# Kernel tuning notes

Hardware: AMD Instinct MI355X
Metric: run time of the kernel (lower is better)

The kernel has to match this reference:

```python
import math
import jax, jax.numpy as jnp
import numpy as np

EPS = 1e-4
FMAX = 18  # max filtersize for scale clamped to 2.5: ceil(3*2^2.5+0.5)=18 -> kernel 37x37
KSZ = 2 * FMAX + 1


def _conv2d(x, w, b):
    # 3x3 conv, padding 1, NCHW / OIHW (cross-correlation, matches torch)
    y = jax.lax.conv_general_dilated(x, w, (1, 1), [(1, 1), (1, 1)],
                                     dimension_numbers=('NCHW', 'OIHW', 'NCHW'))
    return y + b[None, :, None, None]


def _basis_filters(scale):
    # scale: [B] -> [B,3,K,K] (g, dgdx, dgdy), masked to the per-sample support
    std = 2.0 ** scale                              # [B]
    fs = jnp.ceil(3.0 * std + 0.5)                  # per-sample filtersize
    x = jnp.arange(-FMAX, FMAX + 1, dtype=jnp.float32)          # [K]
    m = (jnp.abs(x)[None, :] <= fs[:, None]).astype(jnp.float32)  # [B,K] support mask
    e = jnp.exp(-0.5 * (x[None, :] / std[:, None]) ** 2) * m      # masked 1D gaussian [B,K]
    g = e[:, :, None] * e[:, None, :]                              # [B,K,K]
    g = g / jnp.sum(g, axis=(1, 2), keepdims=True)
    c = (-x[None, :] / (std[:, None] ** 3 * 2.0 * math.pi)) * e    # [B,K]
    dgdx = c[:, :, None] * e[:, None, :]   # varies along first spatial dim (x[0])
    dgdx = dgdx / jnp.sum(jnp.abs(dgdx), axis=(1, 2), keepdims=True)
    dgdy = e[:, :, None] * c[:, None, :]   # varies along second spatial dim (x[1])
    dgdy = dgdy / jnp.sum(jnp.abs(dgdy), axis=(1, 2), keepdims=True)
    return jnp.stack([g, dgdx, dgdy], axis=1)  # [B,3,K,K]


def setup_inputs() -> dict:
    key = jax.random.key(0)
    ks = jax.random.split(key, 7)
    B, H, W = 8, 512, 512
    batch = jax.random.uniform(ks[0], (B, 3, H, W), dtype=jnp.float32)
    gcm = jnp.array([[0.06, 0.63, 0.27], [0.3, 0.04, -0.35], [0.34, -0.6, 0.17]],
                    dtype=jnp.float32)
    w1 = jax.random.normal(ks[1], (16, 3, 3, 3), dtype=jnp.float32) * 0.1
    b1 = jax.random.normal(ks[2], (16,), dtype=jnp.float32) * 0.01
    w2 = jax.random.normal(ks[3], (16, 16, 3, 3), dtype=jnp.float32) * 0.1
    b2 = jax.random.normal(ks[4], (16,), dtype=jnp.float32) * 0.01
    w3 = jax.random.normal(ks[5], (1, 16, 3, 3), dtype=jnp.float32) * 0.1
    b3 = jax.random.normal(ks[6], (1,), dtype=jnp.float32) * 0.01
    return {"batch": batch, "gcm": gcm, "w1": w1, "b1": b1,
            "w2": w2, "b2": b2, "w3": w3, "b3": b3}


def reference(batch, gcm, w1, b1, w2, b2, w3, b3):
    B, _, H, W = batch.shape
    # ---- RGB order prior (non-differentiable, no_grad in torch) ----
    oh = lambda i: jax.nn.one_hot(i, 3, axis=1, dtype=batch.dtype)
    mx = jnp.argmax(batch, axis=1)                 # first max
    mn = jnp.argmin(batch, axis=1)
    bf = batch[:, ::-1]
    mx2 = 2 - jnp.argmax(bf, axis=1)               # last max
    mn2 = 2 - jnp.argmin(bf, axis=1)
    RGB_order = jax.lax.stop_gradient(
        0.5 * (oh(mx) + oh(mx2)) - 0.5 * (oh(mn) + oh(mn2)))  # [B,3,H,W]

    # ---- per-sample adaptive scale from small CNN ----
    h = jax.nn.silu(_conv2d(batch, w1, b1))
    h = jax.nn.silu(_conv2d(h, w2, b2))
    s = _conv2d(h, w3, b3)
    scale = jnp.clip(jnp.mean(s, axis=(1, 2, 3)), -2.5, 2.5)   # [B]

    # ---- Gaussian color model ----
    xg = jnp.einsum('ij,bjhw->bihw', gcm, batch)  # [B,3,H,W] -> (E, El, Ell)

    # ---- per-sample Gaussian basis convolution, batched via grouped conv ----
    basis = _basis_filters(scale)                                  # [B,3,K,K]
    xin = xg.reshape(1, B * 3, H, W)
    wk = jnp.broadcast_to(basis[:, None], (B, 3, 3, KSZ, KSZ)).reshape(B * 9, 1, KSZ, KSZ)
    out = jax.lax.conv_general_dilated(xin, wk, (1, 1), [(FMAX, FMAX), (FMAX, FMAX)],
                                       feature_group_count=B * 3,
                                       dimension_numbers=('NCHW', 'OIHW', 'NCHW'))
    out = out.reshape(B, 3, 3, H, W)   # [B, chan(E/El/Ell), filt(g/dx/dy), H, W]
    E = out[:, 0, 0:1]
    Ex = out[:, 0, 1:2]
    Ey = out[:, 0, 2:3]
    El = out[:, 1, 0:1]
    Ell = out[:, 2, 0:1]

    Hf = jnp.arctan(El / (Ell + EPS))
    S = jnp.log((El ** 2 + Ell ** 2) / (E ** 2 + EPS) + EPS)
    Ww = jnp.arctan((Ex / (E + EPS)) ** 2 + (Ey / (E + EPS)) ** 2)
    return jnp.concatenate([Hf, S, RGB_order, Ww], axis=1)  # [B,6,H,W]
```

## Files before the change

### kernel.cpp

```cpp
#include <hip/hip_runtime.h>
#include <hip/hip_bf16.h>

constexpr int BN = 8, HH = 512, WW = 512;
constexpr int PIX = HH * WW;
constexpr float EPSF = 1e-4f;

__device__ __forceinline__ float b2f(__hip_bfloat16 x) { return __bfloat162float(x); }
__device__ __forceinline__ __hip_bfloat16 f2b(float x) { return __float2bfloat16(x); }
__device__ __forceinline__ unsigned short bfbits(float x) {
    union { __hip_bfloat16 b; unsigned short u; } cv; cv.b = f2b(x); return cv.u;
}

typedef __attribute__((ext_vector_type(8))) short bf16x8;
typedef __attribute__((ext_vector_type(4))) float f32x4;

constexpr int OFF_TOT = 0;
constexpr int OFF_ROW0 = 128;
constexpr int OFF_ROW1 = 256;
constexpr int OFF_COL0 = 384;
constexpr int OFF_COL1 = 512;
constexpr int OFF_COR = 640;
constexpr int OFF_WR  = 2048;
constexpr int OFF_EH  = 4608;
constexpr int OFF_CH  = 5120;
constexpr size_t OFF_TPB = 65536;
constexpr size_t TP_BYTES = (size_t)4 * BN * PIX * 4;
constexpr size_t WS_NEEDED = OFF_TPB + TP_BYTES;

__global__ void prep_kernel(const float* __restrict__ w2, float* __restrict__ wsf) {
    int t = threadIdx.x;
    for (int i = t; i < 640; i += 256) wsf[i] = 0.f;
    unsigned short* ab = (unsigned short*)(wsf + OFF_WR);
    for (int idx = t; idx < 5120; idx += 256) {
        int part = idx / 2560;
        int id = idx - part * 2560;
        int ks = id >> 9, rem = id & 511, lane = rem >> 3, j = id & 7;
        int oc = lane & 15, q = lane >> 4;
        int k = q * 8 + j;
        int tap = 2 * ks + (k >> 4), ic = k & 15;
        float val = (tap <= 8) ? w2[oc * 144 + ic * 9 + tap] : 0.f;
        float hv = b2f(f2b(val));
        ab[idx] = (part == 0) ? bfbits(val) : bfbits(val - hv);
    }
}

__device__ __forceinline__ void conv1_px(const float v[27], const float* __restrict__ w1,
                                         const float* __restrict__ b1, unsigned int u[8]) {
    float o[16];
#pragma unroll
    for (int oc = 0; oc < 16; oc++) {
        float a = b1[oc];
#pragma unroll
        for (int j = 0; j < 27; j++) a += v[j] * w1[oc * 27 + j];
        o[oc] = a / (1.f + __expf(-a));
    }
#pragma unroll
    for (int k = 0; k < 8; k++)
        u[k] = (unsigned int)bfbits(o[2 * k]) | ((unsigned int)bfbits(o[2 * k + 1]) << 16);
}

__global__ __launch_bounds__(256) void conv12_kernel(const float* __restrict__ batch,
                                                     const float* __restrict__ w1,
                                                     const float* __restrict__ b1,
                                                     const unsigned short* __restrict__ abuf,
                                                     const float* __restrict__ b2v,
                                                     const float* __restrict__ gcm,
                                                     float* __restrict__ wsf,
                                                     float* __restrict__ out) {
    __shared__ uint4 h1s[18 * 66 * 2];
    __shared__ float part[4][16];

    int tx = threadIdx.x;
    int lane = tx & 63, wave = tx >> 6;
    int n = lane & 15, q = lane >> 4;
    int w0 = blockIdx.x * 64, h0 = blockIdx.y * 16, b = blockIdx.z;
    bool edge = (blockIdx.x == 0) || (blockIdx.x == 7) || (blockIdx.y == 0) || (blockIdx.y == 31);

    union { uint4 u; bf16x8 v; } cv;
    bf16x8 ah[5], al[5];
    const uint4* ab4 = (const uint4*)abuf;
#pragma unroll
    for (int ks = 0; ks < 5; ks++) {
        cv.u = ab4[ks * 64 + lane];       ah[ks] = cv.v;
        cv.u = ab4[320 + ks * 64 + lane]; al[ks] = cv.v;
    }

    const float* pb = batch + (size_t)(b * 3) * PIX;
    for (int i = tx; i < 18 * 66; i += 256) {
        int r = i / 66, c = i - r * 66;
        int gh = h0 - 1 + r, gw = w0 - 1 + c;
        unsigned int u[8];
        if (!edge) {
            const float* p0 = pb + (size_t)(gh - 1) * WW + (gw - 1);
            float v[27];
#pragma unroll
            for (int ic = 0; ic < 3; ic++)
#pragma unroll
                for (int kh = 0; kh < 3; kh++)
#pragma unroll
                    for (int kw = 0; kw < 3; kw++)
                        v[ic * 9 + kh * 3 + kw] = p0[(size_t)ic * PIX + kh * WW + kw];
            conv1_px(v, w1, b1, u);
        } else if (gh >= 0 && gh < HH && gw >= 0 && gw < WW) {
            float v[27];
#pragma unroll
            for (int ic = 0; ic < 3; ic++) {
                const float* p = pb + (size_t)ic * PIX;
#pragma unroll
                for (int kh = 0; kh < 3; kh++) {
                    int hh = gh + kh - 1;
#pragma unroll
                    for (int kw = 0; kw < 3; kw++) {
                        int ww = gw + kw - 1;
                        float x = 0.f;
                        if (hh >= 0 && hh < HH && ww >= 0 && ww < WW) x = p[hh * WW + ww];
                        v[ic * 9 + kh * 3 + kw] = x;
                    }
                }
            }
            conv1_px(v, w1, b1, u);
        } else {
#pragma unroll
            for (int k = 0; k < 8; k++) u[k] = 0u;
        }
        int swz = (c >> 2) & 1;
        int base = i * 2;
        h1s[base + swz]       = make_uint4(u[0], u[1], u[2], u[3]);
        h1s[base + (swz ^ 1)] = make_uint4(u[4], u[5], u[6], u[7]);
    }

    for (int j = tx; j < 1024; j += 256) {
        int rr = j >> 6, ccx = j & 63;
        size_t p = (size_t)(h0 + rr) * WW + (w0 + ccx);
        float v0 = pb[p], v1 = pb[(size_t)PIX + p], v2 = pb[2 * (size_t)PIX + p];
        int mx  = (v0 >= v1 && v0 >= v2) ? 0 : ((v1 >= v2) ? 1 : 2);
        int mx2 = (v2 >= v1 && v2 >= v0) ? 2 : ((v1 >= v0) ? 1 : 0);
        int mn  = (v0 <= v1 && v0 <= v2) ? 0 : ((v1 <= v2) ? 1 : 2);
        int mn2 = (v2 <= v1 && v2 <= v0) ? 2 : ((v1 <= v0) ? 1 : 0);
#pragma unroll
        for (int c = 0; c < 3; c++) {
            float r = 0.5f * ((float)(c == mx) + (float)(c == mx2))
                    - 0.5f * ((float)(c == mn) + (float)(c == mn2));
            out[(size_t)(b * 6 + 2 + c) * PIX + p] = r;
        }
    }
    __syncthreads();

    float tt[4] = {0, 0, 0, 0};
    float cs0[4] = {0, 0, 0, 0};
    float cs1[4] = {0, 0, 0, 0};
    for (int rloc = 0; rloc < 4; rloc++) {
        int row = wave * 4 + rloc;
        int grow = h0 + row;
        f32x4 acc[4] = {{0,0,0,0},{0,0,0,0},{0,0,0,0},{0,0,0,0}};
#pragma unroll
        for (int ks = 0; ks < 5; ks++) {
            int tap = 2 * ks + (q >> 1); if (tap > 8) tap = 8;
            int dh = tap / 3 - 1, dw = tap % 3 - 1;
            int half = q & 1;
            int lr = row + 1 + dh;
#pragma unroll
            for (int t = 0; t < 4; t++) {
                int c = 1 + dw + t * 16 + n;
                cv.u = h1s[(lr * 66 + c) * 2 + (half ^ ((c >> 2) & 1))];
                acc[t] = __builtin_amdgcn_mfma_f32_16x16x32_bf16(ah[ks], cv.v, acc[t], 0, 0, 0);
                acc[t] = __builtin_amdgcn_mfma_f32_16x16x32_bf16(al[ks], cv.v, acc[t], 0, 0, 0);
            }
        }
        float sv[4][4];
#pragma unroll
        for (int t = 0; t < 4; t++)
#pragma unroll
            for (int r = 0; r < 4; r++) {
                float a = acc[t][r] + b2v[q * 4 + r];
                sv[t][r] = a / (1.f + __expf(-a));
            }
#pragma unroll
        for (int r = 0; r < 4; r++) tt[r] += sv[0][r] + sv[1][r] + sv[2][r] + sv[3][r];
        if (grow == 0 || grow == HH - 1) {
            int off = (grow == 0) ? OFF_ROW0 : OFF_ROW1;
#pragma unroll
            for (int r = 0; r < 4; r++) {
                float x = sv[0][r] + sv[1][r] + sv[2][r] + sv[3][r];
#pragma unroll
                for (int d = 1; d < 16; d <<= 1) x += __shfl_xor(x, d, 64);
                if (n == 0) atomicAdd(&wsf[off + b * 16 + q * 4 + r], x);
            }
        }
        if (blockIdx.x == 0 && n == 0)
#pragma unroll
            for (int r = 0; r < 4; r++) cs0[r] += sv[0][r];
        if (blockIdx.x == 7 && n == 15)
#pragma unroll
            for (int r = 0; r < 4; r++) cs1[r] += sv[3][r];
        if ((grow == 0 || grow == HH - 1)) {
            int hi = (grow == 0) ? 0 : 1;
            if (blockIdx.x == 0 && n == 0)
#pragma unroll
                for (int r = 0; r < 4; r++)
                    wsf[OFF_COR + ((b * 2 + hi) * 2 + 0) * 16 + q * 4 + r] = sv[0][r];
            if (blockIdx.x == 7 && n == 15)
#pragma unroll
                for (int r = 0; r < 4; r++)
                    wsf[OFF_COR + ((b * 2 + hi) * 2 + 1) * 16 + q * 4 + r] = sv[3][r];
        }
    }
    if (blockIdx.x == 0 && n == 0)
#pragma unroll
        for (int r = 0; r < 4; r++) atomicAdd(&wsf[OFF_COL0 + b * 16 + q * 4 + r], cs0[r]);
    if (blockIdx.x == 7 && n == 15)
#pragma unroll
        for (int r = 0; r < 4; r++) atomicAdd(&wsf[OFF_COL1 + b * 16 + q * 4 + r], cs1[r]);
#pragma unroll
    for (int r = 0; r < 4; r++) {
        float x = tt[r];
#pragma unroll
        for (int d = 1; d < 16; d <<= 1) x += __shfl_xor(x, d, 64);
        tt[r] = x;
    }
    if (n == 0)
#pragma unroll
        for (int r = 0; r < 4; r++) part[wave][q * 4 + r] = tt[r];
    __syncthreads();
    if (tx < 16)
        atomicAdd(&wsf[OFF_TOT + b * 16 + tx],
                  part[0][tx] + part[1][tx] + part[2][tx] + part[3][tx]);
}

__global__ void filter_kernel(const float* __restrict__ w3, const float* __restrict__ b3,
                              float* __restrict__ wsf) {
    int b = blockIdx.x, t = threadIdx.x;
    __shared__ float red[160];
    float val = 0.f;
    if (t < 144) {
        int ic = t / 9, tap = t % 9, kh = tap / 3, kw = tap % 3;
        float T = wsf[OFF_TOT + b * 16 + ic];
        int hi = -1, wi = -1;
        if (kh == 0) { T -= wsf[OFF_ROW1 + b * 16 + ic]; hi = 1; }
        else if (kh == 2) { T -= wsf[OFF_ROW0 + b * 16 + ic]; hi = 0; }
        if (kw == 0) { T -= wsf[OFF_COL1 + b * 16 + ic]; wi = 1; }
        else if (kw == 2) { T -= wsf[OFF_COL0 + b * 16 + ic]; wi = 0; }
        if (hi >= 0 && wi >= 0) T += wsf[OFF_COR + ((b * 2 + hi) * 2 + wi) * 16 + ic];
        val = w3[t] * T;
    }
    red[t] = val;
    __syncthreads();
    __shared__ float sh_mean;
    if (t == 0) {
        float S = 0.f;
        for (int i = 0; i < 144; i++) S += red[i];
        sh_mean = b3[0] + S * (1.f / (float)PIX);
    }
    __syncthreads();
    float scale = fminf(2.5f, fmaxf(-2.5f, sh_mean));
    float sd = exp2f(scale);
    float fs = ceilf(3.f * sd + 0.5f);
    float e = 0.f, c = 0.f;
    if (t < 37) {
        float x = (float)(t - 18);
        if (fabsf(x) <= fs) {
            float qq = x / sd;
            e = __expf(-0.5f * qq * qq);
            c = -x / (sd * sd * sd * 6.28318530717958647692f) * e;
        }
    }
    __shared__ float sa[40], sb[40];
    if (t < 37) { sa[t] = e; sb[t] = fabsf(c); }
    __syncthreads();
    __shared__ float Se, Sc;
    if (t == 0) {
        float a = 0.f, d = 0.f;
        for (int i = 0; i < 37; i++) { a += sa[i]; d += sb[i]; }
        Se = a; Sc = d;
    }
    __syncthreads();
    if (t < 37) {
        wsf[OFF_EH + b * 37 + t] = e / Se;
        wsf[OFF_CH + b * 37 + t] = c / Sc;
    }
}

__device__ __forceinline__ int skw(int c) { return c + (c >> 5); }
__global__ __launch_bounds__(256, 4) void horiz_kernel(const float* __restrict__ batch,
                                                       const float* __restrict__ gcm,
                                                       const float* __restrict__ ehat,
                                                       const float* __restrict__ chat,
                                                       float* __restrict__ t) {
    __shared__ float xr[2][3][566];
    int tx = threadIdx.x;
    int h0 = blockIdx.x * 2;
    int b  = blockIdx.y;
    const float* pb = batch + (size_t)(b * 3) * PIX;
    float g0 = gcm[0], g1 = gcm[1], g2 = gcm[2];
    float g3 = gcm[3], g4 = gcm[4], g5 = gcm[5];
    float g6 = gcm[6], g7 = gcm[7], g8 = gcm[8];
    for (int i = tx; i < 2 * 548; i += 256) {
        int r = i / 548, c = i - r * 548;
        int gw = c - 18;
        float v0 = 0.f, v1 = 0.f, v2 = 0.f;
        if (gw >= 0 && gw < WW) {
            size_t p = (size_t)(h0 + r) * WW + gw;
            v0 = pb[p]; v1 = pb[(size_t)PIX + p]; v2 = pb[2 * (size_t)PIX + p];
        }
        int cs = skw(c);
        xr[r][0][cs] = g0 * v0 + g1 * v1 + g2 * v2;
        xr[r][1][cs] = g3 * v0 + g4 * v1 + g5 * v2;
        xr[r][2][cs] = g6 * v0 + g7 * v1 + g8 * v2;
    }
    __syncthreads();
    int r = tx >> 7, colbase = (tx & 127) * 4;
    const float* eh = ehat + b * 37; const float* ch = chat + b * 37;
    float a0[4] = {}, a1[4] = {}, a2[4] = {}, a3[4] = {};
#pragma unroll 4
    for (int kk = 0; kk < 40; kk++) {
        int cs = skw(colbase + kk);
        float x0 = xr[r][0][cs], x1 = xr[r][1][cs], x2 = xr[r][2][cs];
#pragma unroll
        for (int i = 0; i < 4; i++) {
            int k = kk - i;
            if (k >= 0 && k < 37) {
                float ce = eh[k], cc = ch[k];
                a0[i] += ce * x0; a1[i] += ce * x1;
                a2[i] += ce * x2; a3[i] += cc * x0;
            }
        }
    }
    const size_t PL = (size_t)BN * PIX;
    size_t p = (size_t)b * PIX + (size_t)(h0 + r) * WW + colbase;
    *(float4*)&t[0 * PL + p] = make_float4(a0[0], a0[1], a0[2], a0[3]);
    *(float4*)&t[1 * PL + p] = make_float4(a1[0], a1[1], a1[2], a1[3]);
    *(float4*)&t[2 * PL + p] = make_float4(a2[0], a2[1], a2[2], a2[3]);
    *(float4*)&t[3 * PL + p] = make_float4(a3[0], a3[1], a3[2], a3[3]);
}

__global__ __launch_bounds__(256, 4) void vert_kernel(const float* __restrict__ t,
                                                      const float* __restrict__ ehat,
                                                      const float* __restrict__ chat,
                                                      float* __restrict__ out) {
    int tx = threadIdx.x;
    int j = blockIdx.x * 64 + (tx & 63);
    int r0 = (blockIdx.y * 4 + (tx >> 6)) * 4;
    int b = blockIdx.z;
    const float* eh = ehat + b * 37; const float* ch = chat + b * 37;
    const size_t PL = (size_t)BN * PIX;
    const float* t0 = t + (size_t)b * PIX;
    float E[4] = {}, Ex[4] = {}, Ey[4] = {}, El[4] = {}, Ell[4] = {};
#pragma unroll 4
    for (int kk = 0; kk < 40; kk++) {
        int gr = r0 - 18 + kk;
        if (gr >= 0 && gr < HH) {
            size_t idx = (size_t)gr * WW + j;
            float v0 = t0[idx], v1 = t0[PL + idx], v2 = t0[2 * PL + idx], v3 = t0[3 * PL + idx];
#pragma unroll
            for (int i = 0; i < 4; i++) {
                int k = kk - i;
                if (k >= 0 && k < 37) {
                    float ce = eh[k], cc = ch[k];
                    E[i] += ce * v0; Ex[i] += cc * v0; Ey[i] += ce * v3;
                    El[i] += ce * v1; Ell[i] += ce * v2;
                }
            }
        }
    }
#pragma unroll
    for (int i = 0; i < 4; i++) {
        int h = r0 + i;
        float Hf = atanf(El[i] / (Ell[i] + EPSF));
        float S = logf((El[i] * El[i] + Ell[i] * Ell[i]) / (E[i] * E[i] + EPSF) + EPSF);
        float rx = Ex[i] / (E[i] + EPSF), ry = Ey[i] / (E[i] + EPSF);
        float Wv = atanf(rx * rx + ry * ry);
        size_t base = (size_t)(b * 6) * PIX + (size_t)h * WW + j;
        out[base] = Hf;
        out[base + PIX] = S;
        out[base + 5 * (size_t)PIX] = Wv;
    }
}

extern "C" void kernel_launch(void* const* d_in, const int* in_sizes, int n_in,
                              void* d_out, int out_size, void* d_ws, size_t ws_size,
                              hipStream_t stream) {
    const float* batch = (const float*)d_in[0];
    const float* gcm   = (const float*)d_in[1];
    const float* w1    = (const float*)d_in[2];
    const float* b1    = (const float*)d_in[3];
    const float* w2    = (const float*)d_in[4];
    const float* b2    = (const float*)d_in[5];
    const float* w3    = (const float*)d_in[6];
    const float* b3    = (const float*)d_in[7];
    float* out = (float*)d_out;

    if (ws_size < WS_NEEDED) return;

    float* wsf = (float*)d_ws;
    float* tpl = (float*)((char*)d_ws + OFF_TPB);
    float* ehat = wsf + OFF_EH;
    float* chat = wsf + OFF_CH;

    prep_kernel<<<dim3(1), dim3(256), 0, stream>>>(w2, wsf);
    conv12_kernel<<<dim3(8, 32, 8), dim3(256), 0, stream>>>(
        batch, w1, b1, (const unsigned short*)(wsf + OFF_WR), b2, gcm, wsf, out);
    filter_kernel<<<dim3(8), dim3(160), 0, stream>>>(w3, b3, wsf);
    horiz_kernel<<<dim3(256, 8), dim3(256), 0, stream>>>(batch, gcm, ehat, chat, tpl);
    vert_kernel<<<dim3(8, 32, 8), dim3(256), 0, stream>>>(tpl, ehat, chat, out);
}
```

Baseline: 255.6 us.

## Stage input tile in shared memory and halve conv12 row tile

Result: slower. 272.8 us (+6.8%).

```diff
diff --git a/kernel.cpp b/kernel.cpp
--- a/kernel.cpp
+++ b/kernel.cpp
@@ -67,14 +67,14 @@
                                                      const float* __restrict__ gcm,
                                                      float* __restrict__ wsf,
                                                      float* __restrict__ out) {
-    __shared__ uint4 h1s[18 * 66 * 2];
+    __shared__ float st[3][12][68];
+    __shared__ uint4 h1s[10 * 66 * 2];
     __shared__ float part[4][16];
 
     int tx = threadIdx.x;
     int lane = tx & 63, wave = tx >> 6;
     int n = lane & 15, q = lane >> 4;
-    int w0 = blockIdx.x * 64, h0 = blockIdx.y * 16, b = blockIdx.z;
-    bool edge = (blockIdx.x == 0) || (blockIdx.x == 7) || (blockIdx.y == 0) || (blockIdx.y == 31);
+    int w0 = blockIdx.x * 64, h0 = blockIdx.y * 8, b = blockIdx.z;
 
     union { uint4 u; bf16x8 v; } cv;
     bf16x8 ah[5], al[5];
@@ -86,12 +86,24 @@
     }
 
     const float* pb = batch + (size_t)(b * 3) * PIX;
-    for (int i = tx; i < 18 * 66; i += 256) {
+
+    for (int i = tx; i < 2448; i += 256) {
+        int ch = i / 816;
+        int rem = i - ch * 816;
+        int r = rem / 68, c = rem - r * 68;
+        int gh = h0 - 2 + r, gw = w0 - 2 + c;
+        float v = 0.f;
+        if (gh >= 0 && gh < HH && gw >= 0 && gw < WW)
+            v = pb[(size_t)ch * PIX + (size_t)gh * WW + gw];
+        st[ch][r][c] = v;
+    }
+    __syncthreads();
+
+    for (int i = tx; i < 660; i += 256) {
         int r = i / 66, c = i - r * 66;
         int gh = h0 - 1 + r, gw = w0 - 1 + c;
         unsigned int u[8];
-        if (!edge) {
-            const float* p0 = pb + (size_t)(gh - 1) * WW + (gw - 1);
+        if (gh >= 0 && gh < HH && gw >= 0 && gw < WW) {
             float v[27];
 #pragma unroll
             for (int ic = 0; ic < 3; ic++)
@@ -99,25 +111,7 @@
                 for (int kh = 0; kh < 3; kh++)
 #pragma unroll
                     for (int kw = 0; kw < 3; kw++)
-                        v[ic * 9 + kh * 3 + kw] = p0[(size_t)ic * PIX + kh * WW + kw];
-            conv1_px(v, w1, b1, u);
-        } else if (gh >= 0 && gh < HH && gw >= 0 && gw < WW) {
-            float v[27];
-#pragma unroll
-            for (int ic = 0; ic < 3; ic++) {
-                const float* p = pb + (size_t)ic * PIX;
-#pragma unroll
-                for (int kh = 0; kh < 3; kh++) {
-                    int hh = gh + kh - 1;
-#pragma unroll
-                    for (int kw = 0; kw < 3; kw++) {
-                        int ww = gw + kw - 1;
-                        float x = 0.f;
-                        if (hh >= 0 && hh < HH && ww >= 0 && ww < WW) x = p[hh * WW + ww];
-                        v[ic * 9 + kh * 3 + kw] = x;
-                    }
-                }
-            }
+                        v[ic * 9 + kh * 3 + kw] = st[ic][r + kh][c + kw];
             conv1_px(v, w1, b1, u);
         } else {
 #pragma unroll
@@ -129,14 +123,16 @@
         h1s[base + (swz ^ 1)] = make_uint4(u[4], u[5], u[6], u[7]);
     }
 
-    for (int j = tx; j < 1024; j += 256) {
+    for (int j = tx; j < 512; j += 256) {
         int rr = j >> 6, ccx = j & 63;
-        size_t p = (size_t)(h0 + rr) * WW + (w0 + ccx);
-        float v0 = pb[p], v1 = pb[(size_t)PIX + p], v2 = pb[2 * (size_t)PIX + p];
+        float v0 = st[0][rr + 2][ccx + 2];
+        float v1 = st[1][rr + 2][ccx + 2];
+        float v2 = st[2][rr + 2][ccx + 2];
         int mx  = (v0 >= v1 && v0 >= v2) ? 0 : ((v1 >= v2) ? 1 : 2);
         int mx2 = (v2 >= v1 && v2 >= v0) ? 2 : ((v1 >= v0) ? 1 : 0);
         int mn  = (v0 <= v1 && v0 <= v2) ? 0 : ((v1 <= v2) ? 1 : 2);
         int mn2 = (v2 <= v1 && v2 <= v0) ? 2 : ((v1 <= v0) ? 1 : 0);
+        size_t p = (size_t)(h0 + rr) * WW + (w0 + ccx);
 #pragma unroll
         for (int c = 0; c < 3; c++) {
             float r = 0.5f * ((float)(c == mx) + (float)(c == mx2))
@@ -149,8 +145,8 @@
     float tt[4] = {0, 0, 0, 0};
     float cs0[4] = {0, 0, 0, 0};
     float cs1[4] = {0, 0, 0, 0};
-    for (int rloc = 0; rloc < 4; rloc++) {
-        int row = wave * 4 + rloc;
+    for (int rloc = 0; rloc < 2; rloc++) {
+        int row = wave * 2 + rloc;
         int grow = h0 + row;
         f32x4 acc[4] = {{0,0,0,0},{0,0,0,0},{0,0,0,0},{0,0,0,0}};
 #pragma unroll
@@ -397,7 +393,7 @@
     float* chat = wsf + OFF_CH;
 
     prep_kernel<<<dim3(1), dim3(256), 0, stream>>>(w2, wsf);
-    conv12_kernel<<<dim3(8, 32, 8), dim3(256), 0, stream>>>(
+    conv12_kernel<<<dim3(8, 64, 8), dim3(256), 0, stream>>>(
         batch, w1, b1, (const unsigned short*)(wsf + OFF_WR), b2, gcm, wsf, out);
     filter_kernel<<<dim3(8), dim3(160), 0, stream>>>(w3, b3, wsf);
     horiz_kernel<<<dim3(256, 8), dim3(256), 0, stream>>>(batch, gcm, ehat, chat, tpl);
```
